# Performance work log

Hardware: AMD Instinct MI355X
Metric: run time of the kernel (lower is better)

Reference implementation:

```python
import jax, jax.numpy as jnp
import numpy as np

BATCH = 8
MAX_SEQ = 2048
HEAD_NUM = 8
# fixed, deterministic variable lengths (output shape depends on these values,
# so they must be static/compile-time constants)
SEQ_LENGTHS = np.array([2048, 1792, 1536, 1280, 1024, 768, 512, 256], dtype=np.int32)


def setup_inputs() -> dict:
    key = jax.random.key(0)
    # uniform in [0,1) so the >0.5 threshold produces a meaningful bool mask
    attention_mask = jax.random.uniform(key, (BATCH, 1, MAX_SEQ, MAX_SEQ), dtype=jnp.float32)
    return {
        "attention_mask": attention_mask,
        "seq_lengths": SEQ_LENGTHS,
        "head_num": HEAD_NUM,
    }


def reference(attention_mask, seq_lengths, head_num):
    # Faithful to: input_mask = attention_mask.half();
    # npu_gen_attention_mask packs, per batch b, the [:s_b, :s_b] top-left block,
    # repeated head_num times, flattened and concatenated over the batch;
    # then output = packed > 0.5 (bool).
    m = attention_mask.astype(jnp.float16)
    sl = np.asarray(seq_lengths)
    parts = []
    for b in range(sl.shape[0]):  # loop over small fixed batch (ragged sizes)
        s = int(sl[b])
        block = m[b, 0, :s, :s]  # [s, s]
        # repeat over heads without copying until reshape
        parts.append(jnp.broadcast_to(block[None], (head_num, s, s)).reshape(-1))
    packed = jnp.concatenate(parts)  # [head_num * sum(s_b^2)]
    return packed > 0.5
```

## Files before the change

### kernel.cpp

```cpp
#include <hip/hip_runtime.h>
#include <hip/hip_fp16.h>

#define BATCH 8
#define MAX_SEQ 2048
#define HEAD_NUM 8

typedef float vfloat4 __attribute__((ext_vector_type(4)));
typedef int   vint4   __attribute__((ext_vector_type(4)));

__global__ __launch_bounds__(256) void genmask_kernel(
    const float* __restrict__ mask,
    const int*   __restrict__ sl,
    int*         __restrict__ out)
{
    const unsigned int blk = blockIdx.x;

    unsigned long long out_base = 0;
    unsigned int blocks_before = 0;
    unsigned int s = 0;
    int b = 0;
    for (; b < BATCH; ++b) {
        s = (unsigned int)sl[b];
        const unsigned int nb = (HEAD_NUM * (s * s)) >> 10;
        if (blk < blocks_before + nb) break;
        blocks_before += nb;
        out_base += (unsigned long long)HEAD_NUM * s * s;
    }

    const unsigned int local = (blk - blocks_before) * 1024u + threadIdx.x * 4u;
    const unsigned int ss  = s * s;
    const unsigned int h   = local / ss;
    const unsigned int rem = local - h * ss;
    const unsigned int i   = rem / s;
    const unsigned int j   = rem - i * s;

    const vfloat4 v = *(const vfloat4*)(mask
        + (size_t)b * MAX_SEQ * MAX_SEQ
        + (size_t)i * MAX_SEQ + j);

    vint4 r;
    r.x = (__half2float(__float2half(v.x)) > 0.5f) ? 1 : 0;
    r.y = (__half2float(__float2half(v.y)) > 0.5f) ? 1 : 0;
    r.z = (__half2float(__float2half(v.z)) > 0.5f) ? 1 : 0;
    r.w = (__half2float(__float2half(v.w)) > 0.5f) ? 1 : 0;

    __builtin_nontemporal_store(r, (vint4*)(out + out_base + local));
}

extern "C" void kernel_launch(void* const* d_in, const int* in_sizes, int n_in,
                              void* d_out, int out_size, void* d_ws, size_t ws_size,
                              hipStream_t stream) {
    const float* mask = (const float*)d_in[0];
    const int*   sl   = (const int*)d_in[1];
    int*         out  = (int*)d_out;

    const unsigned int n_blocks = (unsigned int)(out_size / 1024);

    genmask_kernel<<<n_blocks, 256, 0, stream>>>(mask, sl, out);
}
```

Measured before the change: 479.7 us.

## Process two chunks per thread with magic-number division and normal stores

Each block now handles 2048 outputs, with each thread doing two vec4 chunks, which halves the number of blocks. The head index is removed by repeated subtraction, and the row index comes from a multiply-shift with a per-length magic constant rather than integer divides. The comparison is done in half precision with __hgt, and the nontemporal store is replaced by a regular store. This cuts per-element index arithmetic and block overhead in a kernel that is bound by memory bandwidth. In exchange it depends on sequence lengths being multiples of 256 and on the magic constants being exact.

```diff
diff --git a/kernel.cpp b/kernel.cpp
--- a/kernel.cpp
+++ b/kernel.cpp
@@ -21,30 +21,53 @@
     int b = 0;
     for (; b < BATCH; ++b) {
         s = (unsigned int)sl[b];
-        const unsigned int nb = (HEAD_NUM * (s * s)) >> 10;
+        const unsigned int nb = (s * s) >> 8;
         if (blk < blocks_before + nb) break;
         blocks_before += nb;
         out_base += (unsigned long long)HEAD_NUM * s * s;
     }
 
-    const unsigned int local = (blk - blocks_before) * 1024u + threadIdx.x * 4u;
-    const unsigned int ss  = s * s;
-    const unsigned int h   = local / ss;
-    const unsigned int rem = local - h * ss;
-    const unsigned int i   = rem / s;
-    const unsigned int j   = rem - i * s;
+    const unsigned int ss = s * s;
+    unsigned int base = (blk - blocks_before) * 2048u;
 
-    const vfloat4 v = *(const vfloat4*)(mask
-        + (size_t)b * MAX_SEQ * MAX_SEQ
-        + (size_t)i * MAX_SEQ + j);
+    unsigned int rem_base = base;
+    #pragma unroll
+    for (int t = 0; t < HEAD_NUM - 1; ++t)
+        if (rem_base >= ss) rem_base -= ss;
 
-    vint4 r;
-    r.x = (__half2float(__float2half(v.x)) > 0.5f) ? 1 : 0;
-    r.y = (__half2float(__float2half(v.y)) > 0.5f) ? 1 : 0;
-    r.z = (__half2float(__float2half(v.z)) > 0.5f) ? 1 : 0;
-    r.w = (__half2float(__float2half(v.w)) > 0.5f) ? 1 : 0;
+    static const unsigned long long Mtab[9] = {
+        0ull,
+        (1ull << 32) + 1,
+        (1ull << 31) + 1,
+        1431655766ull,
+        (1ull << 30) + 1,
+        858993460ull,
+        715827883ull,
+        613566757ull,
+        (1ull << 29) + 1
+    };
+    const unsigned long long M = Mtab[s >> 8];
 
-    __builtin_nontemporal_store(r, (vint4*)(out + out_base + local));
+    const float*  in_b  = mask + (size_t)b * MAX_SEQ * MAX_SEQ;
+    int*          out_p = out + out_base + base;
+    const __half  half_pt5 = __float2half(0.5f);
+
+    #pragma unroll
+    for (int c = 0; c < 2; ++c) {
+        const unsigned int rem = rem_base + c * 1024u + threadIdx.x * 4u;
+        const unsigned int i = (unsigned int)(((unsigned long long)rem * M) >> 40);
+        const unsigned int j = rem - i * s;
+
+        const vfloat4 v = *(const vfloat4*)(in_b + (size_t)i * MAX_SEQ + j);
+
+        vint4 r;
+        r.x = __hgt(__float2half(v.x), half_pt5) ? 1 : 0;
+        r.y = __hgt(__float2half(v.y), half_pt5) ? 1 : 0;
+        r.z = __hgt(__float2half(v.z), half_pt5) ? 1 : 0;
+        r.w = __hgt(__float2half(v.w), half_pt5) ? 1 : 0;
+
+        *(vint4*)(out_p + c * 1024u + threadIdx.x * 4u) = r;
+    }
 }
 
 extern "C" void kernel_launch(void* const* d_in, const int* in_sizes, int n_in,
@@ -54,7 +77,7 @@
     const int*   sl   = (const int*)d_in[1];
     int*         out  = (int*)d_out;
 
-    const unsigned int n_blocks = (unsigned int)(out_size / 1024);
+    const unsigned int n_blocks = (unsigned int)(out_size / 2048);
 
     genmask_kernel<<<n_blocks, 256, 0, stream>>>(mask, sl, out);
 }
```

Measured after the change: 493.8 us. 1.03x slower.

## Use grid-stride persistent blocks with two vectors per thread and magic-number division

Applied to the files above, without the earlier changes.

Replaces the one-block-per-1024-elements launch with a grid capped at 2048 blocks that stride over 2048-element chunks, each thread handling two float4 loads and two int4 stores. Per-batch chunk offsets are precomputed once per block, and the integer divisions for row and column are replaced by a multiply-shift using a table of magic constants indexed by sequence length, which only holds for lengths that are multiples of 256. Head wrap is done by conditional subtraction. The goal is less per-block setup and division cost and more memory-level parallelism on a bandwidth-bound kernel, at the cost of assumptions about the sequence lengths.

```diff
diff --git a/kernel.cpp b/kernel.cpp
--- a/kernel.cpp
+++ b/kernel.cpp
@@ -8,43 +8,76 @@
 typedef float vfloat4 __attribute__((ext_vector_type(4)));
 typedef int   vint4   __attribute__((ext_vector_type(4)));
 
-__global__ __launch_bounds__(256) void genmask_kernel(
+__global__ __launch_bounds__(256, 8) void genmask_kernel(
     const float* __restrict__ mask,
     const int*   __restrict__ sl,
-    int*         __restrict__ out)
+    int*         __restrict__ out,
+    unsigned int n_chunks)
 {
-    const unsigned int blk = blockIdx.x;
+    unsigned int       chunk_start[BATCH + 1];
+    unsigned long long elem_start[BATCH];
+    unsigned int       s_arr[BATCH];
+    unsigned int cs = 0;
+    unsigned long long es = 0;
+    #pragma unroll
+    for (int b = 0; b < BATCH; ++b) {
+        const unsigned int s = (unsigned int)sl[b];
+        s_arr[b] = s;
+        chunk_start[b] = cs;
+        elem_start[b] = es;
+        cs += (s * s) >> 8;
+        es += (unsigned long long)HEAD_NUM * s * s;
+    }
+    chunk_start[BATCH] = cs;
 
-    unsigned long long out_base = 0;
-    unsigned int blocks_before = 0;
-    unsigned int s = 0;
-    int b = 0;
-    for (; b < BATCH; ++b) {
-        s = (unsigned int)sl[b];
-        const unsigned int nb = (HEAD_NUM * (s * s)) >> 10;
-        if (blk < blocks_before + nb) break;
-        blocks_before += nb;
-        out_base += (unsigned long long)HEAD_NUM * s * s;
+    static const unsigned long long Mtab[9] = {
+        0ull, (1ull<<32)+1, (1ull<<31)+1, 1431655766ull, (1ull<<30)+1,
+        858993460ull, 715827883ull, 613566757ull, (1ull<<29)+1 };
+
+    const __half half_pt5 = __float2half(0.5f);
+    const unsigned int t4 = threadIdx.x * 4u;
+
+    for (unsigned int c = blockIdx.x; c < n_chunks; c += gridDim.x) {
+        int b = 0;
+        #pragma unroll
+        for (int t = 1; t < BATCH; ++t)
+            if (c >= chunk_start[t]) b = t;
+        const unsigned int s  = s_arr[b];
+        const unsigned int ss = s * s;
+        const unsigned long long M = Mtab[s >> 8];
+
+        const unsigned int base = (c - chunk_start[b]) * 2048u;
+        unsigned int rem_base = base;
+        #pragma unroll
+        for (int t = 0; t < HEAD_NUM - 1; ++t)
+            if (rem_base >= ss) rem_base -= ss;
+
+        const float* in_b  = mask + (size_t)b * MAX_SEQ * MAX_SEQ;
+        int*         out_p = out + elem_start[b] + base;
+
+        const unsigned int r0 = rem_base + t4;
+        const unsigned int r1 = r0 + 1024u;
+        const unsigned int i0 = (unsigned int)(((unsigned long long)r0 * M) >> 40);
+        const unsigned int i1 = (unsigned int)(((unsigned long long)r1 * M) >> 40);
+        const unsigned int j0 = r0 - i0 * s;
+        const unsigned int j1 = r1 - i1 * s;
+
+        const vfloat4 v0 = *(const vfloat4*)(in_b + (size_t)i0 * MAX_SEQ + j0);
+        const vfloat4 v1 = *(const vfloat4*)(in_b + (size_t)i1 * MAX_SEQ + j1);
+
+        vint4 q0, q1;
+        q0.x = __hgt(__float2half(v0.x), half_pt5) ? 1 : 0;
+        q0.y = __hgt(__float2half(v0.y), half_pt5) ? 1 : 0;
+        q0.z = __hgt(__float2half(v0.z), half_pt5) ? 1 : 0;
+        q0.w = __hgt(__float2half(v0.w), half_pt5) ? 1 : 0;
+        q1.x = __hgt(__float2half(v1.x), half_pt5) ? 1 : 0;
+        q1.y = __hgt(__float2half(v1.y), half_pt5) ? 1 : 0;
+        q1.z = __hgt(__float2half(v1.z), half_pt5) ? 1 : 0;
+        q1.w = __hgt(__float2half(v1.w), half_pt5) ? 1 : 0;
+
+        __builtin_nontemporal_store(q0, (vint4*)(out_p + t4));
+        __builtin_nontemporal_store(q1, (vint4*)(out_p + 1024u + t4));
     }
-
-    const unsigned int local = (blk - blocks_before) * 1024u + threadIdx.x * 4u;
-    const unsigned int ss  = s * s;
-    const unsigned int h   = local / ss;
-    const unsigned int rem = local - h * ss;
-    const unsigned int i   = rem / s;
-    const unsigned int j   = rem - i * s;
-
-    const vfloat4 v = *(const vfloat4*)(mask
-        + (size_t)b * MAX_SEQ * MAX_SEQ
-        + (size_t)i * MAX_SEQ + j);
-
-    vint4 r;
-    r.x = (__half2float(__float2half(v.x)) > 0.5f) ? 1 : 0;
-    r.y = (__half2float(__float2half(v.y)) > 0.5f) ? 1 : 0;
-    r.z = (__half2float(__float2half(v.z)) > 0.5f) ? 1 : 0;
-    r.w = (__half2float(__float2half(v.w)) > 0.5f) ? 1 : 0;
-
-    __builtin_nontemporal_store(r, (vint4*)(out + out_base + local));
 }
 
 extern "C" void kernel_launch(void* const* d_in, const int* in_sizes, int n_in,
@@ -54,7 +87,8 @@
     const int*   sl   = (const int*)d_in[1];
     int*         out  = (int*)d_out;
 
-    const unsigned int n_blocks = (unsigned int)(out_size / 1024);
+    const unsigned int n_chunks = (unsigned int)(out_size / 2048);
+    const unsigned int n_blocks = n_chunks < 2048u ? n_chunks : 2048u;
 
-    genmask_kernel<<<n_blocks, 256, 0, stream>>>(mask, sl, out);
+    genmask_kernel<<<n_blocks, 256, 0, stream>>>(mask, sl, out, n_chunks);
 }
```

Measured after the change: 502.1 us. +4.7%, slower.
